# Kernel optimization log

Measured on AMD Instinct MI355X. Metric: run time of the kernel, lower is better.

## Reference

```python
import jax, jax.numpy as jnp
import numpy as np

N = 8192          # number of prototypes
D = 128           # proto_dim == hidden_dim (residual requires equality)
H = 2             # GAT heads
K = 3             # k_neighbors + 1 (k_neighbors=2 hard-coded in forward)
NEG_SLOPE = 0.2   # PyG GATConv default leaky relu slope
LN_EPS = 1e-5


def setup_inputs() -> dict:
    key = jax.random.key(0)
    ks = jax.random.split(key, 6)
    prototypes = jax.random.normal(ks[0], (N, D), dtype=jnp.float32)
    labels = jax.random.randint(ks[1], (N,), 0, 1024, dtype=jnp.int64)
    # GATConv params: lin maps D -> H*D (concat=False => per-head dim = hidden_dim)
    W = jax.random.normal(ks[2], (D, H * D), dtype=jnp.float32) / np.sqrt(D)
    att_src = jax.random.normal(ks[3], (H, D), dtype=jnp.float32) / np.sqrt(D)
    att_dst = jax.random.normal(ks[4], (H, D), dtype=jnp.float32) / np.sqrt(D)
    bias = jnp.zeros((D,), dtype=jnp.float32)
    gamma = jnp.ones((D,), dtype=jnp.float32)   # LayerNorm weight
    beta = jnp.zeros((D,), dtype=jnp.float32)   # LayerNorm bias
    return {"prototypes": prototypes, "labels": labels, "W": W,
            "att_src": att_src, "att_dst": att_dst, "bias": bias,
            "gamma": gamma, "beta": beta}


def _knn_edges(x):
    # Squared euclidean distances (same ordering as torch.cdist -> same topk indices).
    sq = jnp.sum(x * x, axis=-1)
    d2 = sq[:, None] + sq[None, :] - 2.0 * (x @ x.T)          # [N, N]
    _, idx = jax.lax.top_k(-d2, K)                            # [N, K] smallest dists
    # topk includes self (dist 0); module masks self-edges then GATConv re-adds
    # self loops, so the effective edge set is exactly the topk set -> static E=N*K.
    src = jnp.repeat(jnp.arange(x.shape[0]), K)               # edge source j
    dst = idx.reshape(-1)                                     # edge target i
    return src, dst


def _gat(x, src, dst, W, att_src, att_dst, bias):
    n = x.shape[0]
    xp = (x @ W).reshape(n, H, D)                             # [N, H, C]
    a_s = jnp.sum(xp * att_src[None], axis=-1)                # [N, H]
    a_d = jnp.sum(xp * att_dst[None], axis=-1)                # [N, H]
    e = a_s[src] + a_d[dst]                                   # [E, H]
    e = jax.nn.leaky_relu(e, NEG_SLOPE)
    # segment softmax over incoming edges of each destination node
    m = jax.ops.segment_max(e, dst, num_segments=n)           # [N, H]
    w = jnp.exp(e - m[dst])
    denom = jax.ops.segment_sum(w, dst, num_segments=n)       # [N, H]
    alpha = w / denom[dst]                                    # [E, H]
    msg = alpha[:, :, None] * xp[src]                         # [E, H, C]
    out = jax.ops.segment_sum(msg, dst, num_segments=n)       # [N, H, C]
    return out.mean(axis=1) + bias                            # concat=False -> head mean


def reference(prototypes, labels, W, att_src, att_dst, bias, gamma, beta):
    x = prototypes
    src, dst = _knn_edges(x)
    x_new = _gat(x, src, dst, W, att_src, att_dst, bias)
    mu = jnp.mean(x_new, axis=-1, keepdims=True)
    var = jnp.var(x_new, axis=-1, keepdims=True)
    x_new = (x_new - mu) * jax.lax.rsqrt(var + LN_EPS) * gamma + beta
    x_new = jax.nn.relu(x_new)
    # dropout layers are identity in eval mode
    return x + x_new
```

## Files before the change

### kernel.cpp

```cpp
#include <hip/hip_runtime.h>
#include <hip/hip_bf16.h>
#include <math.h>

#define GN 8192
#define GD 128
#define GH 2
#define GK 3
#define NEG_SLOPE 0.2f
#define LN_EPS 1e-5f

using short8  = __attribute__((ext_vector_type(8)))  short;
using float16 = __attribute__((ext_vector_type(16))) float;
using f32x4   = __attribute__((ext_vector_type(4)))  float;

__device__ __forceinline__ float wred(float v) {
    #pragma unroll
    for (int o = 32; o > 0; o >>= 1) v += __shfl_xor(v, o, 64);
    return v;
}

__device__ __forceinline__ unsigned fenc(float f) {
    unsigned b = __float_as_uint(f);
    return (b & 0x80000000u) ? ~b : (b | 0x80000000u);
}

__device__ __forceinline__ float rawbf2f(unsigned short s) {
    return __uint_as_float(((unsigned)s) << 16);
}
__device__ __forceinline__ unsigned short f2rawbf(float f) {
    __hip_bfloat16 b = __float2bfloat16(f);
    unsigned short r; __builtin_memcpy(&r, &b, 2);
    return r;
}
__device__ __forceinline__ unsigned umin2(unsigned a, unsigned b) { return a < b ? a : b; }
__device__ __forceinline__ unsigned umax2(unsigned a, unsigned b) { return a > b ? a : b; }

__global__ void k_pre(const float* __restrict__ W, const float* __restrict__ att_src,
                      const float* __restrict__ att_dst,
                      unsigned short* __restrict__ Wth, unsigned short* __restrict__ Wtl,
                      float* __restrict__ uvec) {
    __shared__ float vs[128];
    int b = blockIdx.x, t = threadIdx.x;
    if (b < 128) {
        int e = b * 256 + t;
        int d = e >> 8, j = e & 255;
        int h = j >> 7, c = j & 127;
        int k = h * 128 + d;
        float w = W[e];
        unsigned short hi = f2rawbf(w);
        Wth[c * 256 + k] = hi;
        Wtl[c * 256 + k] = f2rawbf(w - rawbf2f(hi));
    } else {
        int bb = b - 128;
        int h = bb & 1;
        const float* v = (bb < 2 ? att_src : att_dst) + h * 128;
        if (t < 128) vs[t] = v[t];
        __syncthreads();
        int d = t >> 1, half = t & 1;
        const float* wr = W + (size_t)d * 256 + h * 128 + half * 64;
        float s = 0.f;
        for (int c = 0; c < 64; c++) s += wr[c] * vs[half * 64 + c];
        s += __shfl_xor(s, 1, 64);
        if (half == 0) uvec[bb * 128 + d] = s;
    }
}

__global__ void k_conv(const float* __restrict__ x, const float* __restrict__ uvec,
                       float* __restrict__ sq,
                       unsigned short* __restrict__ xa, unsigned short* __restrict__ xb,
                       float* __restrict__ a_s, float* __restrict__ a_d,
                       int* __restrict__ cnt, int* __restrict__ curs) {
    int row = blockIdx.x * 4 + (threadIdx.x >> 6);
    int lane = threadIdx.x & 63;
    const float* xr = x + (size_t)row * GD;
    float a0 = xr[lane], a1 = xr[lane + 64];
    float s = wred(a0 * a0 + a1 * a1);
    unsigned short* ar = xa + (size_t)row * 144;
    unsigned short* br = xb + (size_t)row * 144;
    ar[lane] = f2rawbf(-2.f * a0); ar[lane + 64] = f2rawbf(-2.f * a1);
    br[lane] = f2rawbf(a0);        br[lane + 64] = f2rawbf(a1);
    float s0 = wred(a0 * uvec[lane]       + a1 * uvec[64 + lane]);
    float s1 = wred(a0 * uvec[128 + lane] + a1 * uvec[192 + lane]);
    float d0 = wred(a0 * uvec[256 + lane] + a1 * uvec[320 + lane]);
    float d1 = wred(a0 * uvec[384 + lane] + a1 * uvec[448 + lane]);
    if (lane < 16) {
        unsigned short av = 0, bv = 0;
        if (lane == 0)      { av = f2rawbf(s + 512.f); bv = 0x3F80; }
        else if (lane == 1) { float hi = rawbf2f(f2rawbf(s + 512.f));
                              av = f2rawbf(s + 512.f - hi); bv = 0x3F80; }
        ar[128 + lane] = av; br[128 + lane] = bv;
        if (lane == 0) {
            sq[row] = s;
            a_s[row * 2] = s0; a_s[row * 2 + 1] = s1;
            a_d[row * 2] = d0; a_d[row * 2 + 1] = d1;
            cnt[row] = 0; curs[row] = 0;
        }
    }
}

#define STAGE_HALF(buf, rowbase)                                                  \
    do {                                                                          \
        _Pragma("unroll")                                                         \
        for (int s_ = 0; s_ < 5; s_++) {                                          \
            if (s_ < 4 || t < 128) {                                              \
                int q_ = s_ * 256 + t;           \
                int kb_ = q_ >> 6, r_ = q_ & 63;                                  \
                __builtin_amdgcn_global_load_lds(                                 \
                    (const __attribute__((address_space(1))) unsigned*)           \
                        (xa + (size_t)((rowbase) + r_) * 144 + kb_ * 8),          \
                    (__attribute__((address_space(3))) unsigned*)&At[(buf)][q_ * 8],\
                    16, 0, 0);                                                    \
            }                                                                     \
        }                                                                         \
    } while (0)

__launch_bounds__(256, 4)
__global__ void k_gemm_topk(const unsigned short* __restrict__ xa,
                            const unsigned short* __restrict__ xb,
                            unsigned* __restrict__ cand) {
    __shared__ unsigned short At[2][18 * 64 * 8];
    int t = threadIdx.x;
    int w = t >> 6, lane = t & 63, h = lane >> 5, n = lane & 31;
    int col = blockIdx.x * 128 + w * 32 + n;
    int sb = blockIdx.y;
    int rb0 = sb * 512;

    short8 bfrag[9];
    #pragma unroll
    for (int kc = 0; kc < 9; kc++)
        bfrag[kc] = *(const short8*)(xb + (size_t)col * 144 + (2 * kc + h) * 8);

    STAGE_HALF(0, rb0);
    asm volatile("s_waitcnt vmcnt(0)" ::: "memory");
    __builtin_amdgcn_s_barrier();

    unsigned T0 = 0xFFFFFFFFu, T1 = 0xFFFFFFFFu, T2 = 0xFFFFFFFFu, T3 = 0xFFFFFFFFu;

    #pragma unroll 1
    for (int ht = 0; ht < 8; ht++) {
        int cur = ht & 1;
        if (ht < 7) STAGE_HALF(cur ^ 1, rb0 + (ht + 1) * 64);

        float16 acc[2];
        #pragma unroll
        for (int rs = 0; rs < 2; rs++) acc[rs] = (float16)(0.f);

        #pragma unroll
        for (int kc = 0; kc < 9; kc++) {
            short8 a0 = *(const short8*)&At[cur][(((2 * kc + h) * 64) + n) * 8];
            short8 a1 = *(const short8*)&At[cur][(((2 * kc + h) * 64) + 32 + n) * 8];
            acc[0] = __builtin_amdgcn_mfma_f32_32x32x16_bf16(a0, bfrag[kc], acc[0], 0, 0, 0);
            acc[1] = __builtin_amdgcn_mfma_f32_32x32x16_bf16(a1, bfrag[kc], acc[1], 0, 0, 0);
        }

        int rbb = rb0 + ht * 64 + 4 * h;
        #pragma unroll
        for (int rs = 0; rs < 2; rs++) {
            float16 A = acc[rs];
            int rb = rbb + rs * 32;
            #pragma unroll
            for (int q4 = 0; q4 < 4; q4++) {
                unsigned c0 = __float_as_uint(A[q4 * 4 + 0]);
                unsigned c1 = __float_as_uint(A[q4 * 4 + 1]);
                unsigned c2 = __float_as_uint(A[q4 * 4 + 2]);
                unsigned c3 = __float_as_uint(A[q4 * 4 + 3]);
                unsigned qm = umin2(umin2(c0, c1), umin2(c2, c3));
                if ((qm & 0xFFFFE000u) <= T3) {
                    #pragma unroll
                    for (int r = 0; r < 4; r++) {
                        unsigned cv = (r == 0) ? c0 : (r == 1) ? c1 : (r == 2) ? c2 : c3;
                        unsigned k = (cv & 0xFFFFE000u) |
                                     (unsigned)(rb + r + 8 * q4);
                        unsigned m0 = umax2(T0, k);  T0 = umin2(T0, k);
                        unsigned m1 = umax2(T1, m0); T1 = umin2(T1, m0);
                        unsigned m2 = umax2(T2, m1); T2 = umin2(T2, m1);
                        T3 = umin2(T3, m2);
                    }
                }
            }
        }

        if (ht < 7) {
            asm volatile("s_waitcnt vmcnt(0)" ::: "memory");
            __builtin_amdgcn_s_barrier();
        }
    }

    unsigned p0 = (unsigned)__shfl_xor((int)T0, 32), p1 = (unsigned)__shfl_xor((int)T1, 32),
             p2 = (unsigned)__shfl_xor((int)T2, 32), p3 = (unsigned)__shfl_xor((int)T3, 32);
    #pragma unroll
    for (int q = 0; q < 4; q++) {
        unsigned k = (q == 0) ? p0 : (q == 1) ? p1 : (q == 2) ? p2 : p3;
        unsigned m0 = umax2(T0, k);  T0 = umin2(T0, k);
        unsigned m1 = umax2(T1, m0); T1 = umin2(T1, m0);
        unsigned m2 = umax2(T2, m1); T2 = umin2(T2, m1);
        T3 = umin2(T3, m2);
    }
    if (h == 0) {
        uint4 o = make_uint4(T0, T1, T2, T3);
        *(uint4*)(cand + (size_t)col * 64 + sb * 4) = o;
    }
}

__device__ __forceinline__ int clampN(int v) {
    return v < 0 ? 0 : (v >= GN ? GN - 1 : v);
}

__global__ void k_refine(const unsigned* __restrict__ cand,
                         const float* __restrict__ x, const float* __restrict__ sq,
                         int* __restrict__ fidx, int* __restrict__ cnt) {
    int t = threadIdx.x, wv = t >> 6, lane = t & 63;
    int j = blockIdx.x * 4 + wv;
    int c = lane >> 2, g = lane & 3;

    unsigned key32 = cand[(size_t)j * 64 + lane];
    int myidx = 0;
    #pragma unroll
    for (int r = 0; r < 16; r++) {
        unsigned m = key32;
        #pragma unroll
        for (int o = 32; o > 0; o >>= 1)
            m = umin2(m, (unsigned)__shfl_xor((int)m, o, 64));
        myidx = (c == r) ? (int)(m & 8191u) : myidx;
        key32 = (key32 == m) ? 0xFFFFFFFFu : key32;
    }

    const float* xi = x + (size_t)myidx * GD + g * 32;
    const float* xj = x + (size_t)j * GD + g * 32;
    float p = 0.f;
    #pragma unroll
    for (int d4 = 0; d4 < 8; d4++) {
        float4 a = *(const float4*)(xi + d4 * 4);
        float4 b = *(const float4*)(xj + d4 * 4);
        p += a.x * b.x + a.y * b.y + a.z * b.z + a.w * b.w;
    }
    p += __shfl_xor(p, 1, 64);
    p += __shfl_xor(p, 2, 64);
    float d2 = sq[j] + sq[myidx] - 2.f * p;
    unsigned long long key = ((unsigned long long)fenc(d2) << 32) | (unsigned)myidx;

    int out3[3];
    #pragma unroll
    for (int r = 0; r < 3; r++) {
        unsigned long long k = key;
        #pragma unroll
        for (int o = 4; o <= 32; o <<= 1) {
            unsigned long long other = __shfl_xor(k, o, 64);
            k = k < other ? k : other;
        }
        out3[r] = (int)(unsigned)(k & 8191u);
        key = (key == k) ? ~0ull : key;
    }
    if (lane == 0) {
        int i0 = clampN(out3[0]), i1 = clampN(out3[1]), i2 = clampN(out3[2]);
        fidx[j * 3 + 0] = i0; fidx[j * 3 + 1] = i1; fidx[j * 3 + 2] = i2;
        atomicAdd(&cnt[i0], 1); atomicAdd(&cnt[i1], 1); atomicAdd(&cnt[i2], 1);
    }
}

__global__ void k_scan(const int* __restrict__ cnt, int* __restrict__ offs) {
    __shared__ __align__(16) int buf[8192];
    __shared__ int wtot[4];
    int t = threadIdx.x, wv = t >> 6, lane = t & 63;
    #pragma unroll
    for (int j = 0; j < 8; j++)
        ((int4*)buf)[j * 256 + t] = ((const int4*)cnt)[j * 256 + t];
    __syncthreads();
    int loc[32], s = 0;
    #pragma unroll
    for (int k = 0; k < 32; k++) { loc[k] = s; s += buf[t * 32 + k]; }
    int inc = s;
    #pragma unroll
    for (int d = 1; d < 64; d <<= 1) {
        int nv = __shfl_up(inc, d, 64);
        if (lane >= d) inc += nv;
    }
    if (lane == 63) wtot[wv] = inc;
    __syncthreads();
    int wbase = 0;
    #pragma unroll
    for (int wq = 0; wq < 4; wq++) wbase += (wq < wv) ? wtot[wq] : 0;
    int base = wbase + inc - s;
    #pragma unroll
    for (int k = 0; k < 32; k++) buf[t * 32 + k] = base + loc[k];
    __syncthreads();
    #pragma unroll
    for (int j = 0; j < 8; j++)
        ((int4*)offs)[j * 256 + t] = ((int4*)buf)[j * 256 + t];
    if (t == 255) offs[GN] = wtot[0] + wtot[1] + wtot[2] + wtot[3];
}

__global__ void k_fill(const int* __restrict__ fidx, const int* __restrict__ offs,
                       int* __restrict__ cursor, int* __restrict__ elist,
                       const float* __restrict__ a_s, const float* __restrict__ a_d,
                       float2* __restrict__ ew) {
    int eid = blockIdx.x * 256 + threadIdx.x;
    int i = clampN(fidx[eid]);
    int src = eid / 3;
    float2 as = ((const float2*)a_s)[src];
    float2 ad = ((const float2*)a_d)[i];
    float e0 = as.x + ad.x; e0 = e0 >= 0.f ? e0 : NEG_SLOPE * e0;
    float e1 = as.y + ad.y; e1 = e1 >= 0.f ? e1 : NEG_SLOPE * e1;
    float w0 = expf(e0), w1 = expf(e1);
    int pos = atomicAdd(&cursor[i], 1);
    int slot = offs[i] + pos;
    if (slot < GN * GK) { elist[slot] = src; ew[slot] = make_float2(w0, w1); }
}

__launch_bounds__(512, 4)
__global__ void k_out(const int* __restrict__ offs, const int* __restrict__ elst,
                      const float2* __restrict__ ew,
                      const float* __restrict__ x,
                      const unsigned short* __restrict__ Wth,
                      const unsigned short* __restrict__ Wtl,
                      const float* __restrict__ bias, const float* __restrict__ gamma,
                      const float* __restrict__ beta, float* __restrict__ out) {
    __shared__ unsigned short zh[16][264];
    __shared__ unsigned short zl[16][264];
    __shared__ float os[16][132];
    int t = threadIdx.x, i0 = blockIdx.x * 16;
    int wv = t >> 6, lane = t & 63;
    int eslot = lane >> 3, g = lane & 7;

    #pragma unroll
    for (int pp = 0; pp < 2; pp++) {
        int r = wv * 2 + pp, node = i0 + r;
        int s = offs[node], e = offs[node + 1];
        float acc0[16], acc1[16];
        #pragma unroll
        for (int q = 0; q < 16; q++) { acc0[q] = 0.f; acc1[q] = 0.f; }
        float w0s = 0.f, w1s = 0.f;
        for (int k0 = s; k0 < e; k0 += 8) {
            int k = k0 + eslot;
            bool valid = k < e;
            int j = valid ? elst[k] : 0;
            float2 wv2 = valid ? ew[k] : make_float2(0.f, 0.f);
            const float* xr = x + (size_t)j * GD + g * 16;
            float4 x0 = *(const float4*)(xr);
            float4 x1 = *(const float4*)(xr + 4);
            float4 x2 = *(const float4*)(xr + 8);
            float4 x3 = *(const float4*)(xr + 12);
            float xv[16] = {x0.x, x0.y, x0.z, x0.w, x1.x, x1.y, x1.z, x1.w,
                            x2.x, x2.y, x2.z, x2.w, x3.x, x3.y, x3.z, x3.w};
            #pragma unroll
            for (int q = 0; q < 16; q++) {
                acc0[q] += wv2.x * xv[q];
                acc1[q] += wv2.y * xv[q];
            }
            w0s += wv2.x; w1s += wv2.y;
        }
        #pragma unroll
        for (int m = 8; m <= 32; m <<= 1) {
            #pragma unroll
            for (int q = 0; q < 16; q++) {
                acc0[q] += __shfl_xor(acc0[q], m, 64);
                acc1[q] += __shfl_xor(acc1[q], m, 64);
            }
            w0s += __shfl_xor(w0s, m, 64);
            w1s += __shfl_xor(w1s, m, 64);
        }
        if (lane < 8) {
            float dn0 = 0.5f / w0s, dn1 = 0.5f / w1s;
            #pragma unroll
            for (int q = 0; q < 16; q += 2) {
                float a0 = acc0[q] * dn0, a1 = acc0[q + 1] * dn0;
                unsigned short h0 = f2rawbf(a0), h1 = f2rawbf(a1);
                *(unsigned*)&zh[r][lane * 16 + q] = (unsigned)h0 | ((unsigned)h1 << 16);
                *(unsigned*)&zl[r][lane * 16 + q] =
                    (unsigned)f2rawbf(a0 - rawbf2f(h0)) |
                    ((unsigned)f2rawbf(a1 - rawbf2f(h1)) << 16);
                float b0 = acc1[q] * dn1, b1 = acc1[q + 1] * dn1;
                unsigned short p0 = f2rawbf(b0), p1 = f2rawbf(b1);
                *(unsigned*)&zh[r][128 + lane * 16 + q] = (unsigned)p0 | ((unsigned)p1 << 16);
                *(unsigned*)&zl[r][128 + lane * 16 + q] =
                    (unsigned)f2rawbf(b0 - rawbf2f(p0)) |
                    ((unsigned)f2rawbf(b1 - rawbf2f(p1)) << 16);
            }
        }
    }
    __syncthreads();

    {
        int qd = lane >> 4, an = lane & 15;
        int c = wv * 16 + an;
        f32x4 acc = {0.f, 0.f, 0.f, 0.f};
        #pragma unroll
        for (int s = 0; s < 8; s++) {
            int ko = s * 32 + qd * 8;
            short8 ah = *(const short8*)&zh[an][ko];
            short8 al = *(const short8*)&zl[an][ko];
            short8 bh = *(const short8*)(Wth + (size_t)c * 256 + ko);
            short8 bl = *(const short8*)(Wtl + (size_t)c * 256 + ko);
            acc = __builtin_amdgcn_mfma_f32_16x16x32_bf16(ah, bh, acc, 0, 0, 0);
            acc = __builtin_amdgcn_mfma_f32_16x16x32_bf16(al, bh, acc, 0, 0, 0);
            acc = __builtin_amdgcn_mfma_f32_16x16x32_bf16(ah, bl, acc, 0, 0, 0);
        }
        #pragma unroll
        for (int r = 0; r < 4; r++) os[qd * 4 + r][c] = acc[r];
    }
    __syncthreads();

    #pragma unroll
    for (int pp = 0; pp < 2; pp++) {
        int r = wv * 2 + pp, node = i0 + r;
        float y0 = os[r][lane] + bias[lane];
        float y1 = os[r][lane + 64] + bias[lane + 64];
        float mu = wred(y0 + y1) * (1.f / 128.f);
        float c0 = y0 - mu, c1 = y1 - mu;
        float var = wred(c0 * c0 + c1 * c1) * (1.f / 128.f);
        float rs2 = 1.f / sqrtf(var + LN_EPS);
        float n0 = c0 * rs2 * gamma[lane] + beta[lane];
        float n1 = c1 * rs2 * gamma[lane + 64] + beta[lane + 64];
        n0 = n0 > 0.f ? n0 : 0.f;
        n1 = n1 > 0.f ? n1 : 0.f;
        out[(size_t)node * GD + lane]      = x[(size_t)node * GD + lane] + n0;
        out[(size_t)node * GD + lane + 64] = x[(size_t)node * GD + lane + 64] + n1;
    }
}

extern "C" void kernel_launch(void* const* d_in, const int* in_sizes, int n_in,
                              void* d_out, int out_size, void* d_ws, size_t ws_size,
                              hipStream_t stream) {
    const float* x       = (const float*)d_in[0];
    const float* W       = (const float*)d_in[2];
    const float* att_src = (const float*)d_in[3];
    const float* att_dst = (const float*)d_in[4];
    const float* bias    = (const float*)d_in[5];
    const float* gamma   = (const float*)d_in[6];
    const float* beta    = (const float*)d_in[7];
    float* out = (float*)d_out;

    char* w = (char*)d_ws;
    unsigned short* xa = (unsigned short*)w; w += (size_t)GN * 144 * 2;
    unsigned short* xb = (unsigned short*)w; w += (size_t)GN * 144 * 2;
    unsigned* cand = (unsigned*)w;           w += (size_t)GN * 64 * 4;
    float2* ew  = (float2*)w; w += (size_t)GN * GK * 8;
    unsigned short* Wth = (unsigned short*)w; w += (size_t)256 * 128 * 2;
    unsigned short* Wtl = (unsigned short*)w; w += (size_t)256 * 128 * 2;
    float* uvec = (float*)w; w += (size_t)4 * 128 * 4;
    float* sq   = (float*)w; w += (size_t)GN * 4;
    float* a_s  = (float*)w; w += (size_t)GN * GH * 4;
    float* a_d  = (float*)w; w += (size_t)GN * GH * 4;
    int*   fidx = (int*)w;   w += (size_t)GN * GK * 4;
    int*   cnt  = (int*)w;   w += (size_t)GN * 4;
    int*   curs = (int*)w;   w += (size_t)GN * 4;
    int*   offs = (int*)w;   w += (size_t)(GN + 1) * 4;
    int*   elst = (int*)w;   w += (size_t)GN * GK * 4;
    size_t need = (size_t)((char*)w - (char*)d_ws);
    if (ws_size < need) return;

    k_pre<<<132, 256, 0, stream>>>(W, att_src, att_dst, Wth, Wtl, uvec);
    k_conv<<<GN / 4, 256, 0, stream>>>(x, uvec, sq, xa, xb, a_s, a_d, cnt, curs);
    k_gemm_topk<<<dim3(64, 16), 256, 0, stream>>>(xa, xb, cand);
    k_refine<<<GN / 4, 256, 0, stream>>>(cand, x, sq, fidx, cnt);
    k_scan<<<1, 256, 0, stream>>>(cnt, offs);
    k_fill<<<GN * GK / 256, 256, 0, stream>>>(fidx, offs, curs, elst, a_s, a_d, ew);
    k_out<<<GN / 16, 512, 0, stream>>>(offs, elst, ew, x, Wth, Wtl, bias, gamma, beta, out);
}
```

Measured before the change: 169.3 us.

## Retile GEMM-topk warps as 2x2 so each A fragment feeds two column tiles

Each wave previously owned 32 columns and all 64 rows of each staged tile, reading two A fragments per k-step against one B fragment. Waves are now arranged 2x2: each owns 32 rows and 64 columns, loading one A fragment from LDS and reusing it across two register-resident B fragments. This halves LDS reads per MFMA. In exchange it doubles B register footprint and the per-thread top-4 state. It also adds a cross-wave merge through shared memory with an extra barrier at the end.

After: 195.3 us. +15.3%, slower.

```diff
diff --git a/kernel.cpp b/kernel.cpp
--- a/kernel.cpp
+++ b/kernel.cpp
@@ -98,6 +98,28 @@
     }
 }
 
+#define INS(U0,U1,U2,U3,kk) do {                                   \
+    unsigned m0_ = umax2(U0,(kk)); U0 = umin2(U0,(kk));            \
+    unsigned m1_ = umax2(U1,m0_);  U1 = umin2(U1,m0_);             \
+    unsigned m2_ = umax2(U2,m1_);  U2 = umin2(U2,m1_);             \
+    U3 = umin2(U3,m2_); } while(0)
+
+#define TOPK16(A, U0,U1,U2,U3, rbase) do {                                        \
+    _Pragma("unroll")                                                             \
+    for (int q4_ = 0; q4_ < 4; q4_++) {                                           \
+        unsigned c0_ = __float_as_uint((A)[q4_ * 4 + 0]);                         \
+        unsigned c1_ = __float_as_uint((A)[q4_ * 4 + 1]);                         \
+        unsigned c2_ = __float_as_uint((A)[q4_ * 4 + 2]);                         \
+        unsigned c3_ = __float_as_uint((A)[q4_ * 4 + 3]);                         \
+        unsigned qm_ = umin2(umin2(c0_, c1_), umin2(c2_, c3_));                   \
+        if ((qm_ & 0xFFFFE000u) <= U3) {                                          \
+            INS(U0,U1,U2,U3, (c0_ & 0xFFFFE000u) | (unsigned)((rbase) + 0 + 8 * q4_)); \
+            INS(U0,U1,U2,U3, (c1_ & 0xFFFFE000u) | (unsigned)((rbase) + 1 + 8 * q4_)); \
+            INS(U0,U1,U2,U3, (c2_ & 0xFFFFE000u) | (unsigned)((rbase) + 2 + 8 * q4_)); \
+            INS(U0,U1,U2,U3, (c3_ & 0xFFFFE000u) | (unsigned)((rbase) + 3 + 8 * q4_)); \
+        }                                                                         \
+    } } while(0)
+
 #define STAGE_HALF(buf, rowbase)                                                  \
     do {                                                                          \
         _Pragma("unroll")                                                         \
@@ -118,67 +140,46 @@
 __global__ void k_gemm_topk(const unsigned short* __restrict__ xa,
                             const unsigned short* __restrict__ xb,
                             unsigned* __restrict__ cand) {
-    __shared__ unsigned short At[2][18 * 64 * 8];
+    __shared__ __align__(16) unsigned short At[2][18 * 64 * 8];
     int t = threadIdx.x;
     int w = t >> 6, lane = t & 63, h = lane >> 5, n = lane & 31;
-    int col = blockIdx.x * 128 + w * 32 + n;
+    int wn = w & 1, wm = w >> 1;
+    int colA = blockIdx.x * 128 + wn * 64 + n;
+    int colB = colA + 32;
     int sb = blockIdx.y;
     int rb0 = sb * 512;
 
-    short8 bfrag[9];
-    #pragma unroll
-    for (int kc = 0; kc < 9; kc++)
-        bfrag[kc] = *(const short8*)(xb + (size_t)col * 144 + (2 * kc + h) * 8);
+    short8 bfragA[9], bfragB[9];
+    #pragma unroll
+    for (int kc = 0; kc < 9; kc++) {
+        bfragA[kc] = *(const short8*)(xb + (size_t)colA * 144 + (2 * kc + h) * 8);
+        bfragB[kc] = *(const short8*)(xb + (size_t)colB * 144 + (2 * kc + h) * 8);
+    }
 
     STAGE_HALF(0, rb0);
     asm volatile("s_waitcnt vmcnt(0)" ::: "memory");
     __builtin_amdgcn_s_barrier();
 
-    unsigned T0 = 0xFFFFFFFFu, T1 = 0xFFFFFFFFu, T2 = 0xFFFFFFFFu, T3 = 0xFFFFFFFFu;
+    unsigned TA0 = 0xFFFFFFFFu, TA1 = 0xFFFFFFFFu, TA2 = 0xFFFFFFFFu, TA3 = 0xFFFFFFFFu;
+    unsigned TB0 = 0xFFFFFFFFu, TB1 = 0xFFFFFFFFu, TB2 = 0xFFFFFFFFu, TB3 = 0xFFFFFFFFu;
 
     #pragma unroll 1
     for (int ht = 0; ht < 8; ht++) {
         int cur = ht & 1;
         if (ht < 7) STAGE_HALF(cur ^ 1, rb0 + (ht + 1) * 64);
 
-        float16 acc[2];
-        #pragma unroll
-        for (int rs = 0; rs < 2; rs++) acc[rs] = (float16)(0.f);
+        float16 acc0 = (float16)(0.f), acc1 = (float16)(0.f);
 
         #pragma unroll
         for (int kc = 0; kc < 9; kc++) {
-            short8 a0 = *(const short8*)&At[cur][(((2 * kc + h) * 64) + n) * 8];
-            short8 a1 = *(const short8*)&At[cur][(((2 * kc + h) * 64) + 32 + n) * 8];
-            acc[0] = __builtin_amdgcn_mfma_f32_32x32x16_bf16(a0, bfrag[kc], acc[0], 0, 0, 0);
-            acc[1] = __builtin_amdgcn_mfma_f32_32x32x16_bf16(a1, bfrag[kc], acc[1], 0, 0, 0);
-        }
-
-        int rbb = rb0 + ht * 64 + 4 * h;
-        #pragma unroll
-        for (int rs = 0; rs < 2; rs++) {
-            float16 A = acc[rs];
-            int rb = rbb + rs * 32;
-            #pragma unroll
-            for (int q4 = 0; q4 < 4; q4++) {
-                unsigned c0 = __float_as_uint(A[q4 * 4 + 0]);
-                unsigned c1 = __float_as_uint(A[q4 * 4 + 1]);
-                unsigned c2 = __float_as_uint(A[q4 * 4 + 2]);
-                unsigned c3 = __float_as_uint(A[q4 * 4 + 3]);
-                unsigned qm = umin2(umin2(c0, c1), umin2(c2, c3));
-                if ((qm & 0xFFFFE000u) <= T3) {
-                    #pragma unroll
-                    for (int r = 0; r < 4; r++) {
-                        unsigned cv = (r == 0) ? c0 : (r == 1) ? c1 : (r == 2) ? c2 : c3;
-                        unsigned k = (cv & 0xFFFFE000u) |
-                                     (unsigned)(rb + r + 8 * q4);
-                        unsigned m0 = umax2(T0, k);  T0 = umin2(T0, k);
-                        unsigned m1 = umax2(T1, m0); T1 = umin2(T1, m0);
-                        unsigned m2 = umax2(T2, m1); T2 = umin2(T2, m1);
-                        T3 = umin2(T3, m2);
-                    }
-                }
-            }
-        }
+            short8 a = *(const short8*)&At[cur][(((2 * kc + h) * 64) + wm * 32 + n) * 8];
+            acc0 = __builtin_amdgcn_mfma_f32_32x32x16_bf16(a, bfragA[kc], acc0, 0, 0, 0);
+            acc1 = __builtin_amdgcn_mfma_f32_32x32x16_bf16(a, bfragB[kc], acc1, 0, 0, 0);
+        }
+
+        int rbq = rb0 + ht * 64 + wm * 32 + 4 * h;
+        TOPK16(acc0, TA0, TA1, TA2, TA3, rbq);
+        TOPK16(acc1, TB0, TB1, TB2, TB3, rbq);
 
         if (ht < 7) {
             asm volatile("s_waitcnt vmcnt(0)" ::: "memory");
@@ -186,19 +187,33 @@
         }
     }
 
-    unsigned p0 = (unsigned)__shfl_xor((int)T0, 32), p1 = (unsigned)__shfl_xor((int)T1, 32),
-             p2 = (unsigned)__shfl_xor((int)T2, 32), p3 = (unsigned)__shfl_xor((int)T3, 32);
-    #pragma unroll
-    for (int q = 0; q < 4; q++) {
-        unsigned k = (q == 0) ? p0 : (q == 1) ? p1 : (q == 2) ? p2 : p3;
-        unsigned m0 = umax2(T0, k);  T0 = umin2(T0, k);
-        unsigned m1 = umax2(T1, m0); T1 = umin2(T1, m0);
-        unsigned m2 = umax2(T2, m1); T2 = umin2(T2, m1);
-        T3 = umin2(T3, m2);
-    }
-    if (h == 0) {
-        uint4 o = make_uint4(T0, T1, T2, T3);
-        *(uint4*)(cand + (size_t)col * 64 + sb * 4) = o;
+    uint4* mrg = (uint4*)&At[0][0];
+    if (wm == 0) {
+        mrg[(wn * 64 + lane) * 2 + 0] = make_uint4(TA0, TA1, TA2, TA3);
+        mrg[(wn * 64 + lane) * 2 + 1] = make_uint4(TB0, TB1, TB2, TB3);
+    }
+    __syncthreads();
+    if (wm == 1) {
+        uint4 pa = mrg[(wn * 64 + lane) * 2 + 0];
+        uint4 pb = mrg[(wn * 64 + lane) * 2 + 1];
+        INS(TA0,TA1,TA2,TA3, pa.x); INS(TA0,TA1,TA2,TA3, pa.y);
+        INS(TA0,TA1,TA2,TA3, pa.z); INS(TA0,TA1,TA2,TA3, pa.w);
+        INS(TB0,TB1,TB2,TB3, pb.x); INS(TB0,TB1,TB2,TB3, pb.y);
+        INS(TB0,TB1,TB2,TB3, pb.z); INS(TB0,TB1,TB2,TB3, pb.w);
+
+        unsigned q0 = (unsigned)__shfl_xor((int)TA0, 32), q1 = (unsigned)__shfl_xor((int)TA1, 32),
+                 q2 = (unsigned)__shfl_xor((int)TA2, 32), q3 = (unsigned)__shfl_xor((int)TA3, 32);
+        INS(TA0,TA1,TA2,TA3, q0); INS(TA0,TA1,TA2,TA3, q1);
+        INS(TA0,TA1,TA2,TA3, q2); INS(TA0,TA1,TA2,TA3, q3);
+        q0 = (unsigned)__shfl_xor((int)TB0, 32); q1 = (unsigned)__shfl_xor((int)TB1, 32);
+        q2 = (unsigned)__shfl_xor((int)TB2, 32); q3 = (unsigned)__shfl_xor((int)TB3, 32);
+        INS(TB0,TB1,TB2,TB3, q0); INS(TB0,TB1,TB2,TB3, q1);
+        INS(TB0,TB1,TB2,TB3, q2); INS(TB0,TB1,TB2,TB3, q3);
+
+        if (h == 0) {
+            *(uint4*)(cand + (size_t)colA * 64 + sb * 4) = make_uint4(TA0, TA1, TA2, TA3);
+            *(uint4*)(cand + (size_t)colB * 64 + sb * 4) = make_uint4(TB0, TB1, TB2, TB3);
+        }
     }
 }
 
```
